# Performance work log

Measured on AMD Instinct MI355X. Metric: run time of the kernel, lower is better.

Reference implementation:

```python
import jax, jax.numpy as jnp
import numpy as np

DIM = 1024
N_HEADS = 16
HEAD_DIM = DIM // N_HEADS
WINDOW = 64


def setup_inputs() -> dict:
    key = jax.random.key(0)
    k1, k2, k3 = jax.random.split(key, 3)
    B, N = 4, 8192
    x = jax.random.normal(k1, (B, N, DIM), dtype=jnp.float32)
    w_qkv = jax.random.normal(k2, (3 * DIM, DIM), dtype=jnp.float32) * (1.0 / np.sqrt(DIM))
    b_qkv = jnp.zeros((3 * DIM,), dtype=jnp.float32)
    w_proj = jax.random.normal(k3, (DIM, DIM), dtype=jnp.float32) * (1.0 / np.sqrt(DIM))
    b_proj = jnp.zeros((DIM,), dtype=jnp.float32)
    return {"x": x, "w_qkv": w_qkv, "b_qkv": b_qkv, "w_proj": w_proj, "b_proj": b_proj}


def reference(x, w_qkv, b_qkv, w_proj, b_proj):
    B, N, C = x.shape
    H, D, W = N_HEADS, HEAD_DIM, WINDOW
    # qkv projection: torch Linear => x @ W.T + b
    qkv = x @ w_qkv.T + b_qkv                      # [B, N, 3C]
    qkv = qkv.reshape(B, N, 3, H, D).transpose(2, 0, 3, 1, 4)  # [3, B, H, N, D]
    q, k, v = qkv[0], qkv[1], qkv[2]               # each [B, H, N, D]
    n_w = N // W                                    # N chosen divisible by window
    # split sequence into non-overlapping windows (block-diagonal attention)
    qw = q.reshape(B, H, n_w, W, D)
    kw = k.reshape(B, H, n_w, W, D)
    vw = v.reshape(B, H, n_w, W, D)
    scale = 1.0 / np.sqrt(D)
    attn = jnp.einsum('bhnqd,bhnkd->bhnqk', qw, kw) * scale  # [B,H,n_w,W,W]
    attn = jax.nn.softmax(attn, axis=-1)
    out = jnp.einsum('bhnqk,bhnkd->bhnqd', attn, vw)          # [B,H,n_w,W,D]
    out = out.reshape(B, H, N, D).transpose(0, 2, 1, 3).reshape(B, N, C)
    return out @ w_proj.T + b_proj
```

## Files before the change

kernel.cpp:

```cpp
#include <hip/hip_runtime.h>
#include <hip/hip_bf16.h>
#include <cstdint>
#include <cstddef>


typedef __attribute__((ext_vector_type(8))) short short8;
typedef __attribute__((ext_vector_type(4))) float float4v;

static __device__ __forceinline__ void async16(void* lds_p, const void* g) {
  __builtin_amdgcn_global_load_lds((const __attribute__((address_space(1))) void*)g,
                                   (__attribute__((address_space(3))) void*)lds_p,
                                   16, 0, 0);
}

static __device__ __forceinline__ unsigned short f2bf_bits(float x) {
  unsigned int u = __float_as_uint(x);
  unsigned int r = (u + 0x7fffu + ((u >> 16) & 1u)) >> 16;
  return (unsigned short)r;
}

#define S_BARRIER() asm volatile("s_barrier" ::: "memory")
#define WAIT_VM(n)  asm volatile("s_waitcnt vmcnt(" #n ")" ::: "memory")

__global__ __launch_bounds__(256) void cast_f32_to_bf16(
    const float* __restrict__ in, unsigned short* __restrict__ out, int n4) {
  int i = blockIdx.x * 256 + threadIdx.x;
  if (i >= n4) return;
  float4 v = ((const float4*)in)[i];
  ushort4 o;
  o.x = f2bf_bits(v.x); o.y = f2bf_bits(v.y);
  o.z = f2bf_bits(v.z); o.w = f2bf_bits(v.w);
  ((ushort4*)out)[i] = o;
}

template<bool OUT_BF16>
__global__ __launch_bounds__(512, 2) void gemm256(
    const unsigned short* __restrict__ A,
    const unsigned short* __restrict__ B,
    const float* __restrict__ bias,
    void* __restrict__ Cout,
    int M, int N, int K, int ntiles)
{
  extern __shared__ unsigned short lds[];

  const int t    = threadIdx.x;
  const int wave = t >> 6;
  const int lane = t & 63;
  const int lr   = lane & 15;
  const int lq   = lane >> 4;
  const int wm   = wave >> 2;
  const int wn   = wave & 3;

  const int nwg  = gridDim.x;
  const int q8   = nwg >> 3;
  const int wg   = ((int)blockIdx.x & 7) * q8 + ((int)blockIdx.x >> 3);
  const int GM   = 8;
  const int group = wg / (GM * ntiles);
  const int inG   = wg % (GM * ntiles);
  const int bm    = group * GM + (inG % GM);
  const int bn    = inG / GM;

  const int srow = t >> 3;
  const int sswz = ((t & 7) ^ (srow & 7)) << 3;
  const unsigned short* Abase = A + (size_t)(bm * 256 + srow) * K + sswz;
  const unsigned short* Bbase = B + (size_t)(bn * 256 + srow) * K + sswz;
  const int ldsw = wave * 512;

  auto stageA = [&](int kt, int c) {
    async16(lds + (kt & 1) * 16384 + c * 4096 + ldsw,
            Abase + (size_t)(c * 64) * K + kt * 64);
  };
  auto stageB = [&](int kt, int c) {
    async16(lds + 32768 + (kt & 1) * 16384 + c * 4096 + ldsw,
            Bbase + (size_t)(c * 64) * K + kt * 64);
  };

  const int g0 = ((0 + lq) ^ (lr & 7)) << 3;
  const int g1 = ((4 + lq) ^ (lr & 7)) << 3;
  const int arow0 = (wm * 128 + lr) * 64;
  const int brow0 = (wn * 64 + lr) * 64;

  float4v acc[8][4];
  #pragma unroll
  for (int i = 0; i < 8; ++i)
    #pragma unroll
    for (int j = 0; j < 4; ++j) acc[i][j] = (float4v){0.f, 0.f, 0.f, 0.f};

  const int NT = K >> 6;

  #pragma unroll
  for (int c = 0; c < 4; ++c) stageB(0, c);
  #pragma unroll
  for (int c = 0; c < 4; ++c) stageA(0, c);
  #pragma unroll
  for (int c = 0; c < 4; ++c) stageB(1, c);
  WAIT_VM(4);
  S_BARRIER();

  short8 af[4][2], bf[2][2], bf2[2][2];

  for (int kt = 0; kt < NT; ++kt) {
    const int bc = kt & 1;
    int kt1 = kt + 1; if (kt1 == NT) kt1 = 0;
    int kt2 = kt + 2; if (kt2 >= NT) kt2 -= NT;
    const unsigned short* Al = lds + bc * 16384;
    const unsigned short* Bl = lds + 32768 + bc * 16384;

    #pragma unroll
    for (int mf = 0; mf < 4; ++mf) {
      af[mf][0] = *(const short8*)(Al + arow0 + mf * 1024 + g0);
      af[mf][1] = *(const short8*)(Al + arow0 + mf * 1024 + g1);
    }
    #pragma unroll
    for (int nf = 0; nf < 2; ++nf) {
      bf[nf][0] = *(const short8*)(Bl + brow0 + nf * 1024 + g0);
      bf[nf][1] = *(const short8*)(Bl + brow0 + nf * 1024 + g1);
    }
    stageA(kt1, 0); stageA(kt1, 2);
    S_BARRIER();
    __builtin_amdgcn_s_setprio(1);
    #pragma unroll
    for (int mf = 0; mf < 4; ++mf)
      #pragma unroll
      for (int nf = 0; nf < 2; ++nf) {
        acc[mf][nf] = __builtin_amdgcn_mfma_f32_16x16x32_bf16(af[mf][0], bf[nf][0], acc[mf][nf], 0, 0, 0);
        acc[mf][nf] = __builtin_amdgcn_mfma_f32_16x16x32_bf16(af[mf][1], bf[nf][1], acc[mf][nf], 0, 0, 0);
      }
    __builtin_amdgcn_s_setprio(0);
    S_BARRIER();

    #pragma unroll
    for (int nf = 0; nf < 2; ++nf) {
      bf2[nf][0] = *(const short8*)(Bl + brow0 + (2 + nf) * 1024 + g0);
      bf2[nf][1] = *(const short8*)(Bl + brow0 + (2 + nf) * 1024 + g1);
    }
    stageA(kt1, 1); stageA(kt1, 3);
    S_BARRIER();
    __builtin_amdgcn_s_setprio(1);
    #pragma unroll
    for (int mf = 0; mf < 4; ++mf)
      #pragma unroll
      for (int nf = 0; nf < 2; ++nf) {
        acc[mf][2 + nf] = __builtin_amdgcn_mfma_f32_16x16x32_bf16(af[mf][0], bf2[nf][0], acc[mf][2 + nf], 0, 0, 0);
        acc[mf][2 + nf] = __builtin_amdgcn_mfma_f32_16x16x32_bf16(af[mf][1], bf2[nf][1], acc[mf][2 + nf], 0, 0, 0);
      }
    __builtin_amdgcn_s_setprio(0);
    S_BARRIER();

    #pragma unroll
    for (int mf = 0; mf < 4; ++mf) {
      af[mf][0] = *(const short8*)(Al + arow0 + (4 + mf) * 1024 + g0);
      af[mf][1] = *(const short8*)(Al + arow0 + (4 + mf) * 1024 + g1);
    }
    stageB(kt2, 0); stageB(kt2, 1);
    S_BARRIER();
    __builtin_amdgcn_s_setprio(1);
    #pragma unroll
    for (int mf = 0; mf < 4; ++mf)
      #pragma unroll
      for (int nf = 0; nf < 2; ++nf) {
        acc[4 + mf][nf] = __builtin_amdgcn_mfma_f32_16x16x32_bf16(af[mf][0], bf[nf][0], acc[4 + mf][nf], 0, 0, 0);
        acc[4 + mf][nf] = __builtin_amdgcn_mfma_f32_16x16x32_bf16(af[mf][1], bf[nf][1], acc[4 + mf][nf], 0, 0, 0);
      }
    __builtin_amdgcn_s_setprio(0);
    S_BARRIER();

    stageB(kt2, 2); stageB(kt2, 3);
    WAIT_VM(4);
    S_BARRIER();
    __builtin_amdgcn_s_setprio(1);
    #pragma unroll
    for (int mf = 0; mf < 4; ++mf)
      #pragma unroll
      for (int nf = 0; nf < 2; ++nf) {
        acc[4 + mf][2 + nf] = __builtin_amdgcn_mfma_f32_16x16x32_bf16(af[mf][0], bf2[nf][0], acc[4 + mf][2 + nf], 0, 0, 0);
        acc[4 + mf][2 + nf] = __builtin_amdgcn_mfma_f32_16x16x32_bf16(af[mf][1], bf2[nf][1], acc[4 + mf][2 + nf], 0, 0, 0);
      }
    __builtin_amdgcn_s_setprio(0);
    S_BARRIER();
  }

  WAIT_VM(0);

  if (OUT_BF16) {
    unsigned short* Ost = lds + wave * 4096;
    const int cb = bn * 256 + wn * 64;
    #pragma unroll
    for (int p = 0; p < 2; ++p) {
      #pragma unroll
      for (int nf = 0; nf < 4; ++nf) {
        const float bv = bias[cb + nf * 16 + lr];
        #pragma unroll
        for (int mh = 0; mh < 4; ++mh)
          #pragma unroll
          for (int r = 0; r < 4; ++r) {
            const int row = mh * 16 + lq * 4 + r;
            Ost[row * 64 + ((nf * 16 + lr) ^ (lq << 4))] =
                f2bf_bits(acc[p * 4 + mh][nf][r] + bv);
          }
      }
      #pragma unroll
      for (int k = 0; k < 8; ++k) {
        const int cid = k * 64 + lane;
        const int row = cid >> 3;
        const int c8  = cid & 7;
        const int lqr = (row >> 2) & 3;
        short8 v = *(const short8*)(Ost + row * 64 + ((c8 * 8) ^ (lqr << 4)));
        const size_t grow = (size_t)(bm * 256 + wm * 128 + p * 64 + row);
        *(short8*)((unsigned short*)Cout + grow * N + cb + c8 * 8) = v;
      }
    }
  } else {
    const int rbase = bm * 256 + wm * 128 + lq * 4;
    const int cbase = bn * 256 + wn * 64 + lr;
    #pragma unroll
    for (int nf = 0; nf < 4; ++nf) {
      const int col = cbase + nf * 16;
      const float bv = bias[col];
      #pragma unroll
      for (int mf = 0; mf < 8; ++mf) {
        const int row = rbase + mf * 16;
        #pragma unroll
        for (int r = 0; r < 4; ++r)
          ((float*)Cout)[(size_t)(row + r) * N + col] = acc[mf][nf][r] + bv;
      }
    }
  }
}

#define WPB 4

__global__ __launch_bounds__(256) void win_attn(
    const unsigned short* __restrict__ qkv,
    unsigned short* __restrict__ out)
{
  __shared__ unsigned short Qs[2][64 * 64];
  __shared__ unsigned short Ks[2][64 * 64];
  __shared__ unsigned short Vt[2][64 * 64];
  __shared__ unsigned short Ps[64 * 64];

  const int t    = threadIdx.x;
  const int wave = t >> 6;
  const int lane = t & 63;
  const int lr   = lane & 15;
  const int lq   = lane >> 4;
  const int gbase = blockIdx.x * WPB;

  const int srow = t >> 3;
  const int scol = (t & 7) << 3;

  ushort4 vr[2][2];

  for (int i = -1, c = 0; i < WPB; ++i) {
    const int nxt = c ^ 1;
    if (i + 1 < WPB) {
      const int g  = gbase + i + 1;
      const int b  = g >> 11, h = (g >> 7) & 15, wi = g & 127;
      const unsigned short* qb =
          qkv + (size_t)(b * 8192 + wi * 64) * 3072 + h * 64;
      const unsigned short* kb = qb + 1024;
      const unsigned short* vb = qb + 2048;
      const int s = (i + 1) & 1;
      unsigned short* Qw = Qs[s] + wave * 512;
      unsigned short* Kw = Ks[s] + wave * 512;
      #pragma unroll
      for (int o = 0; o < 2; ++o) {
        async16(Qw + o * 2048, qb + (size_t)(o * 32 + srow) * 3072 + scol);
        async16(Kw + o * 2048, kb + (size_t)(o * 32 + srow) * 3072 + scol);
      }
      #pragma unroll
      for (int o = 0; o < 2; ++o) {
        const int d = wave * 8 + o * 32;
        vr[o][0] = *(const ushort4*)(vb + (size_t)lane * 3072 + d);
        vr[o][1] = *(const ushort4*)(vb + (size_t)lane * 3072 + d + 4);
      }
    }

    if (i < 0) {
      #pragma unroll
      for (int o = 0; o < 2; ++o) {
        const int d = wave * 8 + o * 32;
        unsigned short* V = Vt[0];
        V[(d + 0) * 64 + lane] = vr[o][0].x; V[(d + 1) * 64 + lane] = vr[o][0].y;
        V[(d + 2) * 64 + lane] = vr[o][0].z; V[(d + 3) * 64 + lane] = vr[o][0].w;
        V[(d + 4) * 64 + lane] = vr[o][1].x; V[(d + 5) * 64 + lane] = vr[o][1].y;
        V[(d + 6) * 64 + lane] = vr[o][1].z; V[(d + 7) * 64 + lane] = vr[o][1].w;
      }
      __syncthreads();
      continue;
    }

    const int g  = gbase + i;
    const int b  = g >> 11, h = (g >> 7) & 15, wi = g & 127;
    const int tok0 = b * 8192 + wi * 64;

    short8 qa[2];
    #pragma unroll
    for (int k2 = 0; k2 < 2; ++k2)
      qa[k2] = *(const short8*)(Qs[c] + (wave * 16 + lr) * 64 + k2 * 32 + lq * 8);

    float4v s4[4];
    #pragma unroll
    for (int jt = 0; jt < 4; ++jt) {
      float4v a = (float4v){0.f, 0.f, 0.f, 0.f};
      #pragma unroll
      for (int k2 = 0; k2 < 2; ++k2) {
        short8 kf = *(const short8*)(Ks[c] + (jt * 16 + lr) * 64 + k2 * 32 + lq * 8);
        a = __builtin_amdgcn_mfma_f32_16x16x32_bf16(qa[k2], kf, a, 0, 0, 0);
      }
      s4[jt] = a;
    }

    const float scale = 0.125f;
    float pr[4][4];
    #pragma unroll
    for (int r = 0; r < 4; ++r) {
      float m = s4[0][r];
      #pragma unroll
      for (int jt = 1; jt < 4; ++jt) m = fmaxf(m, s4[jt][r]);
      #pragma unroll
      for (int off = 1; off < 16; off <<= 1) m = fmaxf(m, __shfl_xor(m, off));
      float sum = 0.f;
      #pragma unroll
      for (int jt = 0; jt < 4; ++jt) {
        float e = __expf((s4[jt][r] - m) * scale);
        pr[jt][r] = e; sum += e;
      }
      #pragma unroll
      for (int off = 1; off < 16; off <<= 1) sum += __shfl_xor(sum, off);
      float inv = 1.0f / sum;
      #pragma unroll
      for (int jt = 0; jt < 4; ++jt) pr[jt][r] *= inv;
    }

    #pragma unroll
    for (int jt = 0; jt < 4; ++jt)
      #pragma unroll
      for (int r = 0; r < 4; ++r)
        Ps[(wave * 16 + lq * 4 + r) * 64 + jt * 16 + lr] = f2bf_bits(pr[jt][r]);
    __syncthreads();

    short8 pa[2];
    #pragma unroll
    for (int k2 = 0; k2 < 2; ++k2)
      pa[k2] = *(const short8*)(Ps + (wave * 16 + lr) * 64 + k2 * 32 + lq * 8);

    float4v o4[4];
    #pragma unroll
    for (int jd = 0; jd < 4; ++jd) {
      float4v a = (float4v){0.f, 0.f, 0.f, 0.f};
      #pragma unroll
      for (int k2 = 0; k2 < 2; ++k2) {
        short8 vf = *(const short8*)(Vt[c] + (jd * 16 + lr) * 64 + k2 * 32 + lq * 8);
        a = __builtin_amdgcn_mfma_f32_16x16x32_bf16(pa[k2], vf, a, 0, 0, 0);
      }
      o4[jd] = a;
    }

    unsigned short* Ost = Ps + wave * 1024;
    #pragma unroll
    for (int jd = 0; jd < 4; ++jd)
      #pragma unroll
      for (int r = 0; r < 4; ++r)
        Ost[(lq * 4 + r) * 64 + ((jd * 16 + lr) ^ (lq << 4))] =
            f2bf_bits(o4[jd][r]);
    #pragma unroll
    for (int k = 0; k < 2; ++k) {
      const int cid = k * 64 + lane;
      const int row = cid >> 3;
      const int c8  = cid & 7;
      const int lqr = (row >> 2) & 3;
      short8 v = *(const short8*)(Ost + row * 64 + ((c8 * 8) ^ (lqr << 4)));
      *(short8*)(out + (size_t)(tok0 + wave * 16 + row) * 1024 + h * 64 + c8 * 8) = v;
    }

    if (i + 1 < WPB) {
      #pragma unroll
      for (int o = 0; o < 2; ++o) {
        const int d = wave * 8 + o * 32;
        unsigned short* V = Vt[nxt];
        V[(d + 0) * 64 + lane] = vr[o][0].x; V[(d + 1) * 64 + lane] = vr[o][0].y;
        V[(d + 2) * 64 + lane] = vr[o][0].z; V[(d + 3) * 64 + lane] = vr[o][0].w;
        V[(d + 4) * 64 + lane] = vr[o][1].x; V[(d + 5) * 64 + lane] = vr[o][1].y;
        V[(d + 6) * 64 + lane] = vr[o][1].z; V[(d + 7) * 64 + lane] = vr[o][1].w;
      }
    }
    __syncthreads();
    c ^= 1;
  }
}

extern "C" void kernel_launch(void* const* d_in, const int* in_sizes, int n_in,
                              void* d_out, int out_size, void* d_ws, size_t ws_size,
                              hipStream_t stream) {
  const float* x      = (const float*)d_in[0];
  const float* w_qkv  = (const float*)d_in[1];
  const float* b_qkv  = (const float*)d_in[2];
  const float* w_proj = (const float*)d_in[3];
  const float* b_proj = (const float*)d_in[4];
  float* outp = (float*)d_out;

  char* ws = (char*)d_ws;
  unsigned short* xb     = (unsigned short*)(ws);
  unsigned short* wqkvb  = (unsigned short*)(ws + 67108864);
  unsigned short* wprojb = (unsigned short*)(ws + 73400320);
  unsigned short* qkvb   = (unsigned short*)(ws + 75497472);
  unsigned short* attnb  = (unsigned short*)(ws + 276824064);

  static int attr_done = 0;
  if (!attr_done) {
    hipFuncSetAttribute(reinterpret_cast<const void*>(&gemm256<true>),
                        hipFuncAttributeMaxDynamicSharedMemorySize, 131072);
    hipFuncSetAttribute(reinterpret_cast<const void*>(&gemm256<false>),
                        hipFuncAttributeMaxDynamicSharedMemorySize, 131072);
    attr_done = 1;
  }

  cast_f32_to_bf16<<<32768, 256, 0, stream>>>(x,      xb,     33554432 / 4);
  cast_f32_to_bf16<<<3072,  256, 0, stream>>>(w_qkv,  wqkvb,  3145728 / 4);
  cast_f32_to_bf16<<<1024,  256, 0, stream>>>(w_proj, wprojb, 1048576 / 4);

  gemm256<true><<<128 * 12, 512, 131072, stream>>>(xb, wqkvb, b_qkv, qkvb,
                                                   32768, 3072, 1024, 12);
  win_attn<<<8192 / WPB, 256, 0, stream>>>(qkvb, attnb);
  gemm256<false><<<128 * 4, 512, 131072, stream>>>(attnb, wprojb, b_proj, outp,
                                                   32768, 1024, 1024, 4);
}
```

Baseline: 588.1 us.

## Restructure window attention pipeline with XOR-swizzled LDS, register Q, per-wave P

Rewrites the windowed attention kernel so Q is loaded straight into registers instead of staged through LDS. K and V tiles use XOR-swizzled LDS layouts to cut bank conflicts, and the P buffer becomes per-wave, which removes one block barrier per window. It also doubles windows per block, adds an occupancy hint, and replaces __syncthreads with explicit vmcnt/lgkmcnt waits and a raw s_barrier. The hand-written waitcnt counts could become wrong if the compiler reorders the loads, and fewer blocks may reduce parallelism.

Result: no change. 580.0 us (-1.4%).

```diff
diff --git a/kernel.cpp b/kernel.cpp
--- a/kernel.cpp
+++ b/kernel.cpp
@@ -21,6 +21,7 @@
 
 #define S_BARRIER() asm volatile("s_barrier" ::: "memory")
 #define WAIT_VM(n)  asm volatile("s_waitcnt vmcnt(" #n ")" ::: "memory")
+#define WAIT_LGKM0() asm volatile("s_waitcnt lgkmcnt(0)" ::: "memory")
 
 __global__ __launch_bounds__(256) void cast_f32_to_bf16(
     const float* __restrict__ in, unsigned short* __restrict__ out, int n4) {
@@ -228,76 +229,79 @@
   }
 }
 
-#define WPB 4
-
-__global__ __launch_bounds__(256) void win_attn(
+#define WPB 8
+
+__global__ __launch_bounds__(256, 4) void win_attn(
     const unsigned short* __restrict__ qkv,
     unsigned short* __restrict__ out)
 {
-  __shared__ unsigned short Qs[2][64 * 64];
   __shared__ unsigned short Ks[2][64 * 64];
   __shared__ unsigned short Vt[2][64 * 64];
-  __shared__ unsigned short Ps[64 * 64];
+  __shared__ unsigned short Ps[4 * 16 * 64];
 
   const int t    = threadIdx.x;
   const int wave = t >> 6;
   const int lane = t & 63;
   const int lr   = lane & 15;
   const int lq   = lane >> 4;
+  const int k7   = lane & 7;
+  const int kh   = lane >> 3;
+  const int kswz = (k7 ^ kh) << 3;
   const int gbase = blockIdx.x * WPB;
-
-  const int srow = t >> 3;
-  const int scol = (t & 7) << 3;
-
-  ushort4 vr[2][2];
-
-  for (int i = -1, c = 0; i < WPB; ++i) {
-    const int nxt = c ^ 1;
-    if (i + 1 < WPB) {
-      const int g  = gbase + i + 1;
-      const int b  = g >> 11, h = (g >> 7) & 15, wi = g & 127;
-      const unsigned short* qb =
-          qkv + (size_t)(b * 8192 + wi * 64) * 3072 + h * 64;
-      const unsigned short* kb = qb + 1024;
-      const unsigned short* vb = qb + 2048;
-      const int s = (i + 1) & 1;
-      unsigned short* Qw = Qs[s] + wave * 512;
-      unsigned short* Kw = Ks[s] + wave * 512;
-      #pragma unroll
-      for (int o = 0; o < 2; ++o) {
-        async16(Qw + o * 2048, qb + (size_t)(o * 32 + srow) * 3072 + scol);
-        async16(Kw + o * 2048, kb + (size_t)(o * 32 + srow) * 3072 + scol);
-      }
-      #pragma unroll
-      for (int o = 0; o < 2; ++o) {
-        const int d = wave * 8 + o * 32;
-        vr[o][0] = *(const ushort4*)(vb + (size_t)lane * 3072 + d);
-        vr[o][1] = *(const ushort4*)(vb + (size_t)lane * 3072 + d + 4);
-      }
-    }
-
-    if (i < 0) {
-      #pragma unroll
-      for (int o = 0; o < 2; ++o) {
-        const int d = wave * 8 + o * 32;
-        unsigned short* V = Vt[0];
-        V[(d + 0) * 64 + lane] = vr[o][0].x; V[(d + 1) * 64 + lane] = vr[o][0].y;
-        V[(d + 2) * 64 + lane] = vr[o][0].z; V[(d + 3) * 64 + lane] = vr[o][0].w;
-        V[(d + 4) * 64 + lane] = vr[o][1].x; V[(d + 5) * 64 + lane] = vr[o][1].y;
-        V[(d + 6) * 64 + lane] = vr[o][1].z; V[(d + 7) * 64 + lane] = vr[o][1].w;
-      }
-      __syncthreads();
-      continue;
-    }
-
-    const int g  = gbase + i;
-    const int b  = g >> 11, h = (g >> 7) & 15, wi = g & 127;
-    const int tok0 = b * 8192 + wi * 64;
-
-    short8 qa[2];
+  unsigned short* Pst = Ps + wave * 1024;
+
+  short8 qa[2], vr[2];
+
+  auto qptr = [&](int g) {
+    const int b = g >> 11, h = (g >> 7) & 15, wi = g & 127;
+    return qkv + (size_t)(b * 8192 + wi * 64) * 3072 + h * 64;
+  };
+  auto stageK = [&](int s, const unsigned short* kb) {
+    #pragma unroll
+    for (int o = 0; o < 2; ++o)
+      async16(&Ks[s][(wave * 16 + o * 8) * 64],
+              kb + (size_t)(wave * 16 + o * 8 + kh) * 3072 + kswz);
+  };
+  auto loadV = [&](const unsigned short* vb) {
+    #pragma unroll
+    for (int o = 0; o < 2; ++o)
+      vr[o] = *(const short8*)(vb + (size_t)lane * 3072 + wave * 8 + o * 32);
+  };
+  auto loadQ = [&](const unsigned short* qb) {
     #pragma unroll
     for (int k2 = 0; k2 < 2; ++k2)
-      qa[k2] = *(const short8*)(Qs[c] + (wave * 16 + lr) * 64 + k2 * 32 + lq * 8);
+      qa[k2] = *(const short8*)(qb + (size_t)(wave * 16 + lr) * 3072 + k2 * 32 + lq * 8);
+  };
+  auto scatterV = [&](int s) {
+    #pragma unroll
+    for (int o = 0; o < 2; ++o) {
+      const int d = wave * 8 + o * 32;
+      #pragma unroll
+      for (int j = 0; j < 8; ++j)
+        Vt[s][(d + j) * 64 + k7 + ((kh ^ j) << 3)] = vr[o][j];
+    }
+  };
+
+  {
+    const unsigned short* qb0 = qptr(gbase);
+    loadV(qb0 + 2048);
+    stageK(0, qb0 + 1024);
+    loadQ(qb0);
+    scatterV(0);
+    WAIT_VM(2);
+    WAIT_LGKM0();
+    S_BARRIER();
+  }
+
+  for (int i = 0; i < WPB; ++i) {
+    const int c = i & 1;
+    const int g = gbase + i;
+    const int h = (g >> 7) & 15;
+    const int tok0 = ((g >> 11) * 8192) + (g & 127) * 64;
+    const bool more = (i + 1 < WPB);
+    const unsigned short* qb1 = qptr(more ? g + 1 : g);
+
+    if (more) { loadV(qb1 + 2048); stageK(c ^ 1, qb1 + 1024); }
 
     float4v s4[4];
     #pragma unroll
@@ -305,11 +309,14 @@
       float4v a = (float4v){0.f, 0.f, 0.f, 0.f};
       #pragma unroll
       for (int k2 = 0; k2 < 2; ++k2) {
-        short8 kf = *(const short8*)(Ks[c] + (jt * 16 + lr) * 64 + k2 * 32 + lq * 8);
+        short8 kf = *(const short8*)(&Ks[c][(jt * 16 + lr) * 64 +
+                                            (((k2 * 4 + lq) ^ (lr & 7)) << 3)]);
         a = __builtin_amdgcn_mfma_f32_16x16x32_bf16(qa[k2], kf, a, 0, 0, 0);
       }
       s4[jt] = a;
     }
+
+    if (more) loadQ(qb1);
 
     const float scale = 0.125f;
     float pr[4][4];
@@ -336,14 +343,15 @@
     #pragma unroll
     for (int jt = 0; jt < 4; ++jt)
       #pragma unroll
-      for (int r = 0; r < 4; ++r)
-        Ps[(wave * 16 + lq * 4 + r) * 64 + jt * 16 + lr] = f2bf_bits(pr[jt][r]);
-    __syncthreads();
-
+      for (int r = 0; r < 4; ++r) {
+        const int row = lq * 4 + r;
+        const int cu  = (jt * 2 + (lr >> 3)) ^ (row & 7);
+        Pst[row * 64 + (cu << 3) + (lr & 7)] = f2bf_bits(pr[jt][r]);
+      }
     short8 pa[2];
     #pragma unroll
     for (int k2 = 0; k2 < 2; ++k2)
-      pa[k2] = *(const short8*)(Ps + (wave * 16 + lr) * 64 + k2 * 32 + lq * 8);
+      pa[k2] = *(const short8*)(&Pst[lr * 64 + (((k2 * 4 + lq) ^ (lr & 7)) << 3)]);
 
     float4v o4[4];
     #pragma unroll
@@ -351,42 +359,35 @@
       float4v a = (float4v){0.f, 0.f, 0.f, 0.f};
       #pragma unroll
       for (int k2 = 0; k2 < 2; ++k2) {
-        short8 vf = *(const short8*)(Vt[c] + (jd * 16 + lr) * 64 + k2 * 32 + lq * 8);
+        short8 vf = *(const short8*)(&Vt[c][(jd * 16 + lr) * 64 +
+                                            (((k2 * 4 + lq) ^ (lr & 7)) << 3)]);
         a = __builtin_amdgcn_mfma_f32_16x16x32_bf16(pa[k2], vf, a, 0, 0, 0);
       }
       o4[jd] = a;
     }
 
-    unsigned short* Ost = Ps + wave * 1024;
+    if (more) scatterV(c ^ 1);
+
     #pragma unroll
     for (int jd = 0; jd < 4; ++jd)
       #pragma unroll
       for (int r = 0; r < 4; ++r)
-        Ost[(lq * 4 + r) * 64 + ((jd * 16 + lr) ^ (lq << 4))] =
-            f2bf_bits(o4[jd][r]);
+        Pst[(lq * 4 + r) * 64 + ((jd * 16 + lr) ^ (lq << 4))] = f2bf_bits(o4[jd][r]);
     #pragma unroll
     for (int k = 0; k < 2; ++k) {
       const int cid = k * 64 + lane;
       const int row = cid >> 3;
       const int c8  = cid & 7;
       const int lqr = (row >> 2) & 3;
-      short8 v = *(const short8*)(Ost + row * 64 + ((c8 * 8) ^ (lqr << 4)));
+      short8 v = *(const short8*)(&Pst[row * 64 + ((c8 * 8) ^ (lqr << 4))]);
       *(short8*)(out + (size_t)(tok0 + wave * 16 + row) * 1024 + h * 64 + c8 * 8) = v;
     }
 
-    if (i + 1 < WPB) {
-      #pragma unroll
-      for (int o = 0; o < 2; ++o) {
-        const int d = wave * 8 + o * 32;
-        unsigned short* V = Vt[nxt];
-        V[(d + 0) * 64 + lane] = vr[o][0].x; V[(d + 1) * 64 + lane] = vr[o][0].y;
-        V[(d + 2) * 64 + lane] = vr[o][0].z; V[(d + 3) * 64 + lane] = vr[o][0].w;
-        V[(d + 4) * 64 + lane] = vr[o][1].x; V[(d + 5) * 64 + lane] = vr[o][1].y;
-        V[(d + 6) * 64 + lane] = vr[o][1].z; V[(d + 7) * 64 + lane] = vr[o][1].w;
-      }
-    }
-    __syncthreads();
-    c ^= 1;
+    if (more) {
+      WAIT_VM(2);
+      WAIT_LGKM0();
+      S_BARRIER();
+    }
   }
 }
 
```
